# Kernel optimization log

Measured on AMD Instinct MI355X. Metric: run time of the kernel, lower is better.

## Reference

```python
import jax, jax.numpy as jnp
import numpy as np

EPS = 1e-5
NUM_HEADS = 16

def layernorm(x, g, b):
    mu = jnp.mean(x, axis=-1, keepdims=True)
    var = jnp.mean(jnp.square(x - mu), axis=-1, keepdims=True)
    return (x - mu) * jax.lax.rsqrt(var + EPS) * g + b

def setup_inputs() -> dict:
    key = jax.random.key(0)
    ks = jax.random.split(key, 5)
    B, N, C = 2, 2048, 1024
    s_in = 1.0 / np.sqrt(C)
    return {
        "x": jax.random.normal(ks[0], (B, N, C), jnp.float32),
        "ln1_g": jnp.ones((C,), jnp.float32),
        "ln1_b": jnp.zeros((C,), jnp.float32),
        "w_qk": jax.random.normal(ks[1], (C, 2 * C), jnp.float32) * s_in,
        "w_v": jax.random.normal(ks[2], (C, C), jnp.float32) * s_in,
        "ln2_g": jnp.ones((C,), jnp.float32),
        "ln2_b": jnp.zeros((C,), jnp.float32),
        "w_proj": jax.random.normal(ks[3], (C, C), jnp.float32) * s_in,
        "b_proj": jnp.zeros((C,), jnp.float32),
    }

def reference(x, ln1_g, ln1_b, w_qk, w_v, ln2_g, ln2_b, w_proj, b_proj):
    B, N, C = x.shape
    H = NUM_HEADS
    hd = C // H
    scale = hd ** (-0.5)
    xn = layernorm(x, ln1_g, ln1_b)
    # qk: [B,N,2C] -> q,k each [B,H,N,hd]
    qk = (xn @ w_qk).reshape(B, N, 2, H, hd).transpose(2, 0, 3, 1, 4)
    q, k = qk[0], qk[1]
    v = (xn @ w_v).reshape(B, N, H, hd).transpose(0, 2, 1, 3)  # [B,H,N,hd]
    attn = jnp.einsum("bhqd,bhkd->bhqk", q, k) * scale
    attn = jax.nn.softmax(attn, axis=-1)
    out = jnp.einsum("bhqk,bhkd->bhqd", attn, v)  # [B,H,N,hd]
    out = out.transpose(0, 2, 1, 3).reshape(B, N, C)
    out = layernorm(out, ln2_g, ln2_b)
    return out @ w_proj + b_proj
```

## Files before the change

kernel.cpp:

```cpp
#include <hip/hip_runtime.h>
#include <hip/hip_bf16.h>


typedef __attribute__((ext_vector_type(8))) short short8;
typedef __attribute__((ext_vector_type(4))) short short4v;
typedef __attribute__((ext_vector_type(4))) float float4v;
typedef __attribute__((ext_vector_type(4))) unsigned uint4v;

__device__ __forceinline__ unsigned short f2bf(float f) {
    unsigned u = __builtin_bit_cast(unsigned, f);
    return (unsigned short)((u + 0x7FFFu + ((u >> 16) & 1u)) >> 16);
}
__device__ __forceinline__ unsigned packbf2(float lo, float hi) {
    return __builtin_amdgcn_perm(__builtin_bit_cast(unsigned, hi) + 0x8000u,
                                 __builtin_bit_cast(unsigned, lo) + 0x8000u,
                                 0x07060302u);
}
__device__ __forceinline__ void gll16(const unsigned short* g, unsigned short* l) {
    __builtin_amdgcn_global_load_lds(
        (const __attribute__((address_space(1))) unsigned int*)g,
        (__attribute__((address_space(3))) unsigned int*)l, 16, 0, 0);
}

__global__ __launch_bounds__(256) void prep(
    const float* __restrict__ x, const float* __restrict__ g1, const float* __restrict__ b1,
    const float* __restrict__ w_qk, const float* __restrict__ w_v,
    const float* __restrict__ w_proj, const float* __restrict__ g2,
    const float* __restrict__ b2,
    unsigned short* __restrict__ xn, unsigned short* __restrict__ wqkvT,
    unsigned short* __restrict__ wgT, float* __restrict__ u, float* __restrict__ w0) {
    __shared__ float sh[32 * 33];
    const int bid = blockIdx.x, tid = threadIdx.x;
    if (bid < 4096) {
        const float4 v = reinterpret_cast<const float4*>(x + (size_t)bid * 1024)[tid];
        float s  = v.x + v.y + v.z + v.w;
        float sq = v.x * v.x + v.y * v.y + v.z * v.z + v.w * v.w;
#pragma unroll
        for (int off = 32; off >= 1; off >>= 1) {
            s  += __shfl_xor(s, off, 64);
            sq += __shfl_xor(sq, off, 64);
        }
        const int w = tid >> 6, lane = tid & 63;
        if (lane == 0) { sh[w] = s; sh[4 + w] = sq; }
        __syncthreads();
        s  = sh[0] + sh[1] + sh[2] + sh[3];
        sq = sh[4] + sh[5] + sh[6] + sh[7];
        const float mu = s * (1.f / 1024.f);
        const float rstd = rsqrtf(sq * (1.f / 1024.f) - mu * mu + 1e-5f);
        const float4 gv = reinterpret_cast<const float4*>(g1)[tid];
        const float4 bv = reinterpret_cast<const float4*>(b1)[tid];
        ushort4 o;
        o.x = f2bf((v.x - mu) * rstd * gv.x + bv.x);
        o.y = f2bf((v.y - mu) * rstd * gv.y + bv.y);
        o.z = f2bf((v.z - mu) * rstd * gv.z + bv.z);
        o.w = f2bf((v.w - mu) * rstd * gv.w + bv.w);
        *reinterpret_cast<ushort4*>(&xn[(size_t)bid * 1024 + tid * 4]) = o;
    } else {
        const float* in; unsigned short* out; int Cc, bx, by; bool doU = false;
        if (bid < 6144)      { int t = bid - 4096; in = w_qk;   out = wqkvT;               Cc = 2048; bx = t & 63; by = t >> 6; }
        else if (bid < 7168) { int t = bid - 6144; in = w_v;    out = wqkvT + 2048 * 1024; Cc = 1024; bx = t & 31; by = t >> 5; }
        else                 { int t = bid - 7168; in = w_proj; out = wgT; doU = true;     Cc = 1024; bx = t & 31; by = t >> 5; }
        const int c0 = bx * 32, r0 = by * 32;
        const int tx = tid & 31, ty = tid >> 5;
#pragma unroll
        for (int i = 0; i < 32; i += 8)
            sh[(ty + i) * 33 + tx] = in[(size_t)(r0 + ty + i) * Cc + c0 + tx];
        __syncthreads();
        const float scale = doU ? g2[r0 + tx] : 1.f;
        const float b2v   = doU ? b2[r0 + tx] : 0.f;
#pragma unroll
        for (int i = 0; i < 32; i += 8) {
            const float raw = sh[tx * 33 + ty + i];
            const float sc  = raw * scale;
            out[(size_t)(c0 + ty + i) * 1024 + r0 + tx] = f2bf(sc);
            if (doU) {
                float pu = sc, pw = raw * b2v;
#pragma unroll
                for (int off = 1; off <= 16; off <<= 1) {
                    pu += __shfl_xor(pu, off, 64);
                    pw += __shfl_xor(pw, off, 64);
                }
                if (tx == 0) {
                    atomicAdd(&u[c0 + ty + i], pu);
                    atomicAdd(&w0[c0 + ty + i], pw);
                }
            }
        }
    }
}

__global__ __launch_bounds__(512) void gemm256_qkv(const unsigned short* __restrict__ A,
                                                   const unsigned short* __restrict__ Bt,
                                                   unsigned short* __restrict__ qb,
                                                   unsigned short* __restrict__ kb,
                                                   unsigned short* __restrict__ vT) {
    __shared__ unsigned short As[2 * 256 * 64], Bs[2 * 256 * 64];
    const int tid = threadIdx.x, lane = tid & 63, w = tid >> 6;
    const int wm = (w >> 2) * 128, wn = (w & 3) * 64;
    const int quad = lane >> 4, l16 = lane & 15;
    const int ls = lane >> 3, sg = lane & 7;
    const int m0 = blockIdx.y * 256, n0 = blockIdx.x * 256;

    float4v acc[8][4];
#pragma unroll
    for (int mi = 0; mi < 8; mi++)
#pragma unroll
        for (int ni = 0; ni < 4; ni++) acc[mi][ni] = float4v{0.f, 0.f, 0.f, 0.f};

    const int g = (sg ^ ls) * 8;
#pragma unroll 1
    for (int s = -1; s < 16; s++) {
        if (s >= 0) __syncthreads();
        if (s + 1 < 16) {
            const int k0 = (s + 1) << 6, buf = ((s + 1) & 1) << 14;
            unsigned short* Ad = As + buf;
            unsigned short* Bd = Bs + buf;
#pragma unroll
            for (int i = 0; i < 4; i++) {
                const int r = w * 32 + i * 8 + ls;
                gll16(&A[(size_t)(m0 + r) * 1024 + k0 + g], &Ad[(w * 32 + i * 8) * 64]);
                gll16(&Bt[(size_t)(n0 + r) * 1024 + k0 + g], &Bd[(w * 32 + i * 8) * 64]);
            }
        }
        if (s < 0) continue;
        const unsigned short* Ac = As + ((s & 1) << 14);
        const unsigned short* Bc = Bs + ((s & 1) << 14);
#pragma unroll
        for (int ks = 0; ks < 2; ks++) {
            short8 af[8], bfr[4];
#pragma unroll
            for (int mi = 0; mi < 8; mi++) {
                const int r = wm + mi * 16 + l16;
                af[mi] = *reinterpret_cast<const short8*>(
                    &Ac[r * 64 + ((ks * 4 + quad) ^ (r & 7)) * 8]);
            }
#pragma unroll
            for (int ni = 0; ni < 4; ni++) {
                const int r = wn + ni * 16 + l16;
                bfr[ni] = *reinterpret_cast<const short8*>(
                    &Bc[r * 64 + ((ks * 4 + quad) ^ (r & 7)) * 8]);
            }
#pragma unroll
            for (int mi = 0; mi < 8; mi++)
#pragma unroll
                for (int ni = 0; ni < 4; ni++)
                    acc[mi][ni] = __builtin_amdgcn_mfma_f32_16x16x32_bf16(
                        af[mi], bfr[ni], acc[mi][ni], 0, 0, 0);
        }
    }

    const float QSCALE = 0.125f * 1.4426950408889634f;
#pragma unroll
    for (int mi = 0; mi < 8; mi++) {
        const int row0 = m0 + wm + mi * 16 + quad * 4;
        const int b = row0 >> 11, nq = row0 & 2047;
#pragma unroll
        for (int ni = 0; ni < 4; ni++) {
            const int col = n0 + wn + ni * 16 + l16;
            if (col < 1024) {
                const int h = col >> 6, d = col & 63;
#pragma unroll
                for (int r = 0; r < 4; r++)
                    qb[(((size_t)b * 16 + h) * 2048 + nq + r) * 64 + d] =
                        f2bf(acc[mi][ni][r] * QSCALE);
            } else if (col < 2048) {
                const int c = col - 1024, h = c >> 6, d = c & 63;
#pragma unroll
                for (int r = 0; r < 4; r++)
                    kb[(((size_t)b * 16 + h) * 2048 + nq + r) * 64 + d] = f2bf(acc[mi][ni][r]);
            } else {
                const int c = col - 2048, h = c >> 6, d = c & 63;
                const short4v sv = {(short)f2bf(acc[mi][ni][0]), (short)f2bf(acc[mi][ni][1]),
                                    (short)f2bf(acc[mi][ni][2]), (short)f2bf(acc[mi][ni][3])};
                *reinterpret_cast<short4v*>(
                    &vT[(((size_t)b * 16 + h) * 64 + d) * 2048 + nq]) = sv;
            }
        }
    }
}

__global__ __launch_bounds__(256) void flash_attn(const unsigned short* __restrict__ qbuf,
                                                  const unsigned short* __restrict__ kb,
                                                  const unsigned short* __restrict__ vT,
                                                  unsigned short* __restrict__ attn,
                                                  float2* __restrict__ part) {
    __shared__ unsigned short Ks[2][64 * 64];
    const int tid = threadIdx.x, lane = tid & 63, w = tid >> 6;
    const int quad = lane >> 4, l16 = lane & 15;
    const int ls = lane >> 3, sg = lane & 7;
    const int q0 = blockIdx.x * 128, bh = blockIdx.y;
    const size_t nbase = (size_t)bh * 2048;

    int srow[2];
#pragma unroll
    for (int i = 0; i < 2; i++) {
        const int pr = w * 16 + i * 8 + ls;
        srow[i] = (pr & 32) | ((pr & 12) << 1) | ((pr & 16) >> 2) | (pr & 3);
    }
    const int sgran = (sg ^ ls) << 3;

    short8 bq[2][2];
#pragma unroll
    for (int q2 = 0; q2 < 2; q2++)
#pragma unroll
        for (int ks = 0; ks < 2; ks++)
            bq[q2][ks] = *reinterpret_cast<const short8*>(
                &qbuf[(nbase + q0 + w * 32 + q2 * 16 + l16) * 64 + ks * 32 + quad * 8]);

    float l_part[2] = {0.f, 0.f};
    float4v o_acc[2][4];
#pragma unroll
    for (int q2 = 0; q2 < 2; q2++)
#pragma unroll
        for (int db = 0; db < 4; db++) o_acc[q2][db] = float4v{0.f, 0.f, 0.f, 0.f};

#pragma unroll
    for (int i = 0; i < 2; i++)
        gll16(&kb[(nbase + srow[i]) * 64 + sgran], &Ks[0][(w * 16 + i * 8) * 64]);

#pragma unroll 1
    for (int s = 0; s < 32; s++) {
        const int kt0 = s << 6;
        __syncthreads();
        if (s + 1 < 32) {
            const int ktn = (s + 1) << 6;
#pragma unroll
            for (int i = 0; i < 2; i++)
                gll16(&kb[(nbase + ktn + srow[i]) * 64 + sgran],
                      &Ks[(s + 1) & 1][(w * 16 + i * 8) * 64]);
        }
        short8 va[2][4];
#pragma unroll
        for (int k2 = 0; k2 < 2; k2++)
#pragma unroll
            for (int db = 0; db < 4; db++)
                va[k2][db] = *reinterpret_cast<const short8*>(
                    &vT[((size_t)bh * 64 + db * 16 + l16) * 2048 + kt0 + k2 * 32 + quad * 8]);

        const unsigned short* Kc = Ks[s & 1];
        short8 kf[2][4];
#pragma unroll
        for (int ks = 0; ks < 2; ks++)
#pragma unroll
            for (int cb = 0; cb < 4; cb++) {
                const int r = cb * 16 + l16;
                kf[ks][cb] = *reinterpret_cast<const short8*>(
                    &Kc[r * 64 + ((ks * 4 + quad) ^ (r & 7)) * 8]);
            }

#pragma unroll
        for (int q2 = 0; q2 < 2; q2++) {
            float4v s_acc[4];
#pragma unroll
            for (int cb = 0; cb < 4; cb++) s_acc[cb] = float4v{0.f, 0.f, 0.f, 0.f};
#pragma unroll
            for (int ks = 0; ks < 2; ks++)
#pragma unroll
                for (int cb = 0; cb < 4; cb++)
                    s_acc[cb] = __builtin_amdgcn_mfma_f32_16x16x32_bf16(
                        kf[ks][cb], bq[q2][ks], s_acc[cb], 0, 0, 0);

            float ls2 = 0.f;
            short8 pb[2];
#pragma unroll
            for (int k2 = 0; k2 < 2; k2++) {
                float p[8];
#pragma unroll
                for (int cc = 0; cc < 2; cc++)
#pragma unroll
                    for (int r = 0; r < 4; r++) {
                        const float pv = __builtin_amdgcn_exp2f(s_acc[k2 * 2 + cc][r]);
                        p[cc * 4 + r] = pv;
                        ls2 += pv;
                    }
                uint4v pd;
                pd.x = packbf2(p[0], p[1]); pd.y = packbf2(p[2], p[3]);
                pd.z = packbf2(p[4], p[5]); pd.w = packbf2(p[6], p[7]);
                pb[k2] = __builtin_bit_cast(short8, pd);
            }
            l_part[q2] += ls2;
#pragma unroll
            for (int k2 = 0; k2 < 2; k2++)
#pragma unroll
                for (int db = 0; db < 4; db++)
                    o_acc[q2][db] = __builtin_amdgcn_mfma_f32_16x16x32_bf16(
                        va[k2][db], pb[k2], o_acc[q2][db], 0, 0, 0);
        }
    }

    const int b = bh >> 4, h = bh & 15;
#pragma unroll
    for (int q2 = 0; q2 < 2; q2++) {
        float lr = l_part[q2];
        lr += __shfl_xor(lr, 16, 64);
        lr += __shfl_xor(lr, 32, 64);
        const float inv = 1.f / lr;
        const int grow = b * 2048 + q0 + w * 32 + q2 * 16 + l16;
        float s = 0.f, s2 = 0.f;
#pragma unroll
        for (int db = 0; db < 4; db++) {
            const float o0 = o_acc[q2][db][0] * inv, o1 = o_acc[q2][db][1] * inv;
            const float o2 = o_acc[q2][db][2] * inv, o3 = o_acc[q2][db][3] * inv;
            const ushort4 st = {f2bf(o0), f2bf(o1), f2bf(o2), f2bf(o3)};
            *reinterpret_cast<ushort4*>(
                &attn[(size_t)grow * 1024 + h * 64 + db * 16 + quad * 4]) = st;
            s  += (o0 + o1) + (o2 + o3);
            s2 += (o0 * o0 + o1 * o1) + (o2 * o2 + o3 * o3);
        }
        s  += __shfl_xor(s, 16, 64);  s  += __shfl_xor(s, 32, 64);
        s2 += __shfl_xor(s2, 16, 64); s2 += __shfl_xor(s2, 32, 64);
        if (quad == 0) part[(size_t)grow * 16 + h] = float2{s, s2};
    }
}

__device__ __forceinline__ void stage_tiles(const unsigned short* __restrict__ A,
                                            const unsigned short* __restrict__ Bt,
                                            int K, int m0, int n0, int k0,
                                            unsigned short* As, unsigned short* Bs,
                                            int w, int ls, int sg) {
#pragma unroll
    for (int i = 0; i < 4; i++) {
        const int r = w * 32 + i * 8 + ls;
        const int g = (sg ^ ls) * 8;
        gll16(&A[(size_t)(m0 + r) * K + k0 + g], &As[(w * 32 + i * 8) * 64]);
        gll16(&Bt[(size_t)(n0 + r) * K + k0 + g], &Bs[(w * 32 + i * 8) * 64]);
    }
}

__device__ __forceinline__ void gemm128_core(const unsigned short* __restrict__ A,
                                             const unsigned short* __restrict__ Bt,
                                             int K, int m0, int n0,
                                             unsigned short* As, unsigned short* Bs,
                                             float4v acc[4][4]) {
    const int tid = threadIdx.x, lane = tid & 63, w = tid >> 6;
    const int wr = (w >> 1) * 64, wc = (w & 1) * 64;
    const int quad = lane >> 4, l16 = lane & 15;
    const int ls = lane >> 3, sg = lane & 7;
#pragma unroll
    for (int mi = 0; mi < 4; mi++)
#pragma unroll
        for (int ni = 0; ni < 4; ni++) acc[mi][ni] = float4v{0.f, 0.f, 0.f, 0.f};

    const int NS = K >> 6;
    stage_tiles(A, Bt, K, m0, n0, 0, As, Bs, w, ls, sg);
    for (int s = 0; s < NS; s++) {
        __syncthreads();
        const int cur = (s & 1) << 13;
        if (s + 1 < NS)
            stage_tiles(A, Bt, K, m0, n0, (s + 1) << 6,
                        As + (((s + 1) & 1) << 13), Bs + (((s + 1) & 1) << 13),
                        w, ls, sg);
        const unsigned short* Ac = As + cur;
        const unsigned short* Bc = Bs + cur;
#pragma unroll
        for (int ks = 0; ks < 2; ks++) {
            short8 af[4], bfr[4];
#pragma unroll
            for (int mi = 0; mi < 4; mi++) {
                const int r = wr + mi * 16 + l16;
                af[mi] = *reinterpret_cast<const short8*>(
                    &Ac[r * 64 + ((ks * 4 + quad) ^ (r & 7)) * 8]);
            }
#pragma unroll
            for (int ni = 0; ni < 4; ni++) {
                const int r = wc + ni * 16 + l16;
                bfr[ni] = *reinterpret_cast<const short8*>(
                    &Bc[r * 64 + ((ks * 4 + quad) ^ (r & 7)) * 8]);
            }
#pragma unroll
            for (int mi = 0; mi < 4; mi++)
#pragma unroll
                for (int ni = 0; ni < 4; ni++)
                    acc[mi][ni] = __builtin_amdgcn_mfma_f32_16x16x32_bf16(
                        af[mi], bfr[ni], acc[mi][ni], 0, 0, 0);
        }
    }
}

__global__ __launch_bounds__(256) void gemm128_proj(const unsigned short* __restrict__ A,
                                                    const unsigned short* __restrict__ Bt,
                                                    const float2* __restrict__ part,
                                                    const float* __restrict__ u,
                                                    const float* __restrict__ w0,
                                                    const float* __restrict__ bias,
                                                    float* __restrict__ out) {
    __shared__ unsigned short As[2 * 128 * 64], Bs[2 * 128 * 64];
    __shared__ float2 rstat_s[128];
    const int m0 = blockIdx.y * 128, n0 = blockIdx.x * 128;
    {
        const int t = threadIdx.x, rloc = t >> 1, half = t & 1;
        const float4* p4 = reinterpret_cast<const float4*>(part);
        float s = 0.f, s2 = 0.f;
#pragma unroll
        for (int j = 0; j < 4; j++) {
            const float4 p = p4[(size_t)(m0 + rloc) * 8 + half * 4 + j];
            s += p.x + p.z; s2 += p.y + p.w;
        }
        s  += __shfl_xor(s, 1, 64);
        s2 += __shfl_xor(s2, 1, 64);
        if (!half) {
            const float mu = s * (1.f / 1024.f);
            const float rstd = rsqrtf(s2 * (1.f / 1024.f) - mu * mu + 1e-5f);
            rstat_s[rloc] = float2{rstd, mu * rstd};
        }
    }
    float4v acc[4][4];
    gemm128_core(A, Bt, 1024, m0, n0, As, Bs, acc);
    const int lane = threadIdx.x & 63, w = threadIdx.x >> 6;
    const int wr = (w >> 1) * 64, wc = (w & 1) * 64;
    const int quad = lane >> 4, l16 = lane & 15;
#pragma unroll
    for (int mi = 0; mi < 4; mi++) {
        const int rl0 = wr + mi * 16 + quad * 4;
        float2 rs[4];
#pragma unroll
        for (int r = 0; r < 4; r++) rs[r] = rstat_s[rl0 + r];
#pragma unroll
        for (int ni = 0; ni < 4; ni++) {
            const int col = n0 + wc + ni * 16 + l16;
            const float uu = u[col], ww = w0[col] + bias[col];
#pragma unroll
            for (int r = 0; r < 4; r++)
                out[(size_t)(m0 + rl0 + r) * 1024 + col] =
                    fmaf(rs[r].x, acc[mi][ni][r], ww - rs[r].y * uu);
        }
    }
}

extern "C" void kernel_launch(void* const* d_in, const int* in_sizes, int n_in,
                              void* d_out, int out_size, void* d_ws, size_t ws_size,
                              hipStream_t stream) {
    const float* x      = (const float*)d_in[0];
    const float* ln1_g  = (const float*)d_in[1];
    const float* ln1_b  = (const float*)d_in[2];
    const float* w_qk   = (const float*)d_in[3];
    const float* w_v    = (const float*)d_in[4];
    const float* ln2_g  = (const float*)d_in[5];
    const float* ln2_b  = (const float*)d_in[6];
    const float* w_proj = (const float*)d_in[7];
    const float* b_proj = (const float*)d_in[8];
    float* out = (float*)d_out;

    char* ws = (char*)d_ws;
    unsigned short* xn      = (unsigned short*)(ws + 0);
    unsigned short* wqkvT   = (unsigned short*)(ws + 8388608);
    unsigned short* wgT     = (unsigned short*)(ws + 14680064);
    unsigned short* qbuf    = (unsigned short*)(ws + 16777216);
    unsigned short* kbuf    = (unsigned short*)(ws + 25165824);
    unsigned short* vTbuf   = (unsigned short*)(ws + 33554432);
    unsigned short* attn    = (unsigned short*)(ws + 41943040);
    float2*         part    = (float2*)(ws + 50331648);
    float*          u       = (float*)(ws + 50888704);
    float*          w0      = (float*)(ws + 50892800);

    hipMemsetAsync(ws + 50888704, 0, 8192, stream);
    prep<<<8192, 256, 0, stream>>>(x, ln1_g, ln1_b, w_qk, w_v, w_proj, ln2_g, ln2_b,
                                   xn, wqkvT, wgT, u, w0);
    gemm256_qkv<<<dim3(12, 16), 512, 0, stream>>>(xn, wqkvT, qbuf, kbuf, vTbuf);
    flash_attn<<<dim3(16, 32), 256, 0, stream>>>(qbuf, kbuf, vTbuf, attn, part);
    gemm128_proj<<<dim3(8, 32), 256, 0, stream>>>(attn, wgT, part, u, w0, b_proj, out);
}
```

Measured before the change: 230.0 us.

## Stage V tiles in LDS for flash attention and retile projection GEMM

The flash attention kernel now loads V tiles into LDS through async global-to-LDS copies with a swizzled layout, as it already did for K. It processes two 64-key sub-tiles per barrier, so there are 16 iterations instead of 32. This replaces per-iteration uncoalesced direct global loads of V and halves the synchronisation count, at the cost of four times the LDS per block. The projection GEMM switches to 128x64 tiles, which doubles the grid to 512 blocks for better CU occupancy. The p row-sum is also reassociated into a tree.

```diff
diff --git a/kernel.cpp b/kernel.cpp
--- a/kernel.cpp
+++ b/kernel.cpp
@@ -184,7 +184,8 @@
                                                   const unsigned short* __restrict__ vT,
                                                   unsigned short* __restrict__ attn,
                                                   float2* __restrict__ part) {
-    __shared__ unsigned short Ks[2][64 * 64];
+    __shared__ unsigned short Ks[2][2][64 * 64];
+    __shared__ unsigned short Vs[2][2][64 * 64];
     const int tid = threadIdx.x, lane = tid & 63, w = tid >> 6;
     const int quad = lane >> 4, l16 = lane & 15;
     const int ls = lane >> 3, sg = lane & 7;
@@ -215,76 +216,91 @@
         for (int db = 0; db < 4; db++) o_acc[q2][db] = float4v{0.f, 0.f, 0.f, 0.f};
 
 #pragma unroll
-    for (int i = 0; i < 2; i++)
-        gll16(&kb[(nbase + srow[i]) * 64 + sgran], &Ks[0][(w * 16 + i * 8) * 64]);
+    for (int t = 0; t < 2; t++)
+#pragma unroll
+        for (int i = 0; i < 2; i++) {
+            gll16(&kb[(nbase + t * 64 + srow[i]) * 64 + sgran],
+                  &Ks[0][t][(w * 16 + i * 8) * 64]);
+            gll16(&vT[((size_t)bh * 64 + w * 16 + i * 8 + ls) * 2048 + t * 64 + sgran],
+                  &Vs[0][t][(w * 16 + i * 8) * 64]);
+        }
 
 #pragma unroll 1
-    for (int s = 0; s < 32; s++) {
-        const int kt0 = s << 6;
+    for (int s = 0; s < 16; s++) {
         __syncthreads();
-        if (s + 1 < 32) {
-            const int ktn = (s + 1) << 6;
-#pragma unroll
-            for (int i = 0; i < 2; i++)
-                gll16(&kb[(nbase + ktn + srow[i]) * 64 + sgran],
-                      &Ks[(s + 1) & 1][(w * 16 + i * 8) * 64]);
-        }
-        short8 va[2][4];
-#pragma unroll
-        for (int k2 = 0; k2 < 2; k2++)
-#pragma unroll
-            for (int db = 0; db < 4; db++)
-                va[k2][db] = *reinterpret_cast<const short8*>(
-                    &vT[((size_t)bh * 64 + db * 16 + l16) * 2048 + kt0 + k2 * 32 + quad * 8]);
-
-        const unsigned short* Kc = Ks[s & 1];
-        short8 kf[2][4];
-#pragma unroll
-        for (int ks = 0; ks < 2; ks++)
-#pragma unroll
-            for (int cb = 0; cb < 4; cb++) {
-                const int r = cb * 16 + l16;
-                kf[ks][cb] = *reinterpret_cast<const short8*>(
-                    &Kc[r * 64 + ((ks * 4 + quad) ^ (r & 7)) * 8]);
-            }
-
-#pragma unroll
-        for (int q2 = 0; q2 < 2; q2++) {
-            float4v s_acc[4];
-#pragma unroll
-            for (int cb = 0; cb < 4; cb++) s_acc[cb] = float4v{0.f, 0.f, 0.f, 0.f};
+        if (s + 1 < 16) {
+            const int ktn = (s + 1) << 7, buf = (s + 1) & 1;
+#pragma unroll
+            for (int t = 0; t < 2; t++)
+#pragma unroll
+                for (int i = 0; i < 2; i++) {
+                    gll16(&kb[(nbase + ktn + t * 64 + srow[i]) * 64 + sgran],
+                          &Ks[buf][t][(w * 16 + i * 8) * 64]);
+                    gll16(&vT[((size_t)bh * 64 + w * 16 + i * 8 + ls) * 2048 + ktn + t * 64 + sgran],
+                          &Vs[buf][t][(w * 16 + i * 8) * 64]);
+                }
+        }
+#pragma unroll
+        for (int t = 0; t < 2; t++) {
+            const unsigned short* Kc = Ks[s & 1][t];
+            const unsigned short* Vc = Vs[s & 1][t];
+
+            short8 kf[2][4];
 #pragma unroll
             for (int ks = 0; ks < 2; ks++)
 #pragma unroll
-                for (int cb = 0; cb < 4; cb++)
-                    s_acc[cb] = __builtin_amdgcn_mfma_f32_16x16x32_bf16(
-                        kf[ks][cb], bq[q2][ks], s_acc[cb], 0, 0, 0);
-
-            float ls2 = 0.f;
-            short8 pb[2];
-#pragma unroll
-            for (int k2 = 0; k2 < 2; k2++) {
-                float p[8];
-#pragma unroll
-                for (int cc = 0; cc < 2; cc++)
-#pragma unroll
-                    for (int r = 0; r < 4; r++) {
-                        const float pv = __builtin_amdgcn_exp2f(s_acc[k2 * 2 + cc][r]);
-                        p[cc * 4 + r] = pv;
-                        ls2 += pv;
-                    }
-                uint4v pd;
-                pd.x = packbf2(p[0], p[1]); pd.y = packbf2(p[2], p[3]);
-                pd.z = packbf2(p[4], p[5]); pd.w = packbf2(p[6], p[7]);
-                pb[k2] = __builtin_bit_cast(short8, pd);
-            }
-            l_part[q2] += ls2;
+                for (int cb = 0; cb < 4; cb++) {
+                    const int r = cb * 16 + l16;
+                    kf[ks][cb] = *reinterpret_cast<const short8*>(
+                        &Kc[r * 64 + ((ks * 4 + quad) ^ (r & 7)) * 8]);
+                }
+            short8 va[2][4];
 #pragma unroll
             for (int k2 = 0; k2 < 2; k2++)
 #pragma unroll
-                for (int db = 0; db < 4; db++)
-                    o_acc[q2][db] = __builtin_amdgcn_mfma_f32_16x16x32_bf16(
-                        va[k2][db], pb[k2], o_acc[q2][db], 0, 0, 0);
+                for (int db = 0; db < 4; db++) {
+                    const int r = db * 16 + l16;
+                    va[k2][db] = *reinterpret_cast<const short8*>(
+                        &Vc[r * 64 + ((k2 * 4 + quad) ^ (r & 7)) * 8]);
+                }
+
+#pragma unroll
+            for (int q2 = 0; q2 < 2; q2++) {
+                float4v s_acc[4];
+#pragma unroll
+                for (int cb = 0; cb < 4; cb++) s_acc[cb] = float4v{0.f, 0.f, 0.f, 0.f};
+#pragma unroll
+                for (int ks = 0; ks < 2; ks++)
+#pragma unroll
+                    for (int cb = 0; cb < 4; cb++)
+                        s_acc[cb] = __builtin_amdgcn_mfma_f32_16x16x32_bf16(
+                            kf[ks][cb], bq[q2][ks], s_acc[cb], 0, 0, 0);
+
+                float ls2 = 0.f;
+                short8 pb[2];
+#pragma unroll
+                for (int k2 = 0; k2 < 2; k2++) {
+                    float p[8];
+#pragma unroll
+                    for (int cc = 0; cc < 2; cc++)
+#pragma unroll
+                        for (int r = 0; r < 4; r++)
+                            p[cc * 4 + r] = __builtin_amdgcn_exp2f(s_acc[k2 * 2 + cc][r]);
+                    ls2 += ((p[0] + p[1]) + (p[2] + p[3])) +
+                           ((p[4] + p[5]) + (p[6] + p[7]));
+                    uint4v pd;
+                    pd.x = packbf2(p[0], p[1]); pd.y = packbf2(p[2], p[3]);
+                    pd.z = packbf2(p[4], p[5]); pd.w = packbf2(p[6], p[7]);
+                    pb[k2] = __builtin_bit_cast(short8, pd);
+                }
+                l_part[q2] += ls2;
+#pragma unroll
+                for (int k2 = 0; k2 < 2; k2++)
+#pragma unroll
+                    for (int db = 0; db < 4; db++)
+                        o_acc[q2][db] = __builtin_amdgcn_mfma_f32_16x16x32_bf16(
+                            va[k2][db], pb[k2], o_acc[q2][db], 0, 0, 0);
+            }
         }
     }
 
@@ -313,82 +329,22 @@
     }
 }
 
-__device__ __forceinline__ void stage_tiles(const unsigned short* __restrict__ A,
-                                            const unsigned short* __restrict__ Bt,
-                                            int K, int m0, int n0, int k0,
-                                            unsigned short* As, unsigned short* Bs,
-                                            int w, int ls, int sg) {
-#pragma unroll
-    for (int i = 0; i < 4; i++) {
-        const int r = w * 32 + i * 8 + ls;
-        const int g = (sg ^ ls) * 8;
-        gll16(&A[(size_t)(m0 + r) * K + k0 + g], &As[(w * 32 + i * 8) * 64]);
-        gll16(&Bt[(size_t)(n0 + r) * K + k0 + g], &Bs[(w * 32 + i * 8) * 64]);
-    }
-}
-
-__device__ __forceinline__ void gemm128_core(const unsigned short* __restrict__ A,
-                                             const unsigned short* __restrict__ Bt,
-                                             int K, int m0, int n0,
-                                             unsigned short* As, unsigned short* Bs,
-                                             float4v acc[4][4]) {
+__global__ __launch_bounds__(256) void gemm_proj(const unsigned short* __restrict__ A,
+                                                 const unsigned short* __restrict__ Bt,
+                                                 const float2* __restrict__ part,
+                                                 const float* __restrict__ u,
+                                                 const float* __restrict__ w0,
+                                                 const float* __restrict__ bias,
+                                                 float* __restrict__ out) {
+    __shared__ unsigned short As[2 * 128 * 64];
+    __shared__ unsigned short Bs[2 * 64 * 64];
+    __shared__ float2 rstat_s[128];
     const int tid = threadIdx.x, lane = tid & 63, w = tid >> 6;
-    const int wr = (w >> 1) * 64, wc = (w & 1) * 64;
     const int quad = lane >> 4, l16 = lane & 15;
     const int ls = lane >> 3, sg = lane & 7;
-#pragma unroll
-    for (int mi = 0; mi < 4; mi++)
-#pragma unroll
-        for (int ni = 0; ni < 4; ni++) acc[mi][ni] = float4v{0.f, 0.f, 0.f, 0.f};
-
-    const int NS = K >> 6;
-    stage_tiles(A, Bt, K, m0, n0, 0, As, Bs, w, ls, sg);
-    for (int s = 0; s < NS; s++) {
-        __syncthreads();
-        const int cur = (s & 1) << 13;
-        if (s + 1 < NS)
-            stage_tiles(A, Bt, K, m0, n0, (s + 1) << 6,
-                        As + (((s + 1) & 1) << 13), Bs + (((s + 1) & 1) << 13),
-                        w, ls, sg);
-        const unsigned short* Ac = As + cur;
-        const unsigned short* Bc = Bs + cur;
-#pragma unroll
-        for (int ks = 0; ks < 2; ks++) {
-            short8 af[4], bfr[4];
-#pragma unroll
-            for (int mi = 0; mi < 4; mi++) {
-                const int r = wr + mi * 16 + l16;
-                af[mi] = *reinterpret_cast<const short8*>(
-                    &Ac[r * 64 + ((ks * 4 + quad) ^ (r & 7)) * 8]);
-            }
-#pragma unroll
-            for (int ni = 0; ni < 4; ni++) {
-                const int r = wc + ni * 16 + l16;
-                bfr[ni] = *reinterpret_cast<const short8*>(
-                    &Bc[r * 64 + ((ks * 4 + quad) ^ (r & 7)) * 8]);
-            }
-#pragma unroll
-            for (int mi = 0; mi < 4; mi++)
-#pragma unroll
-                for (int ni = 0; ni < 4; ni++)
-                    acc[mi][ni] = __builtin_amdgcn_mfma_f32_16x16x32_bf16(
-                        af[mi], bfr[ni], acc[mi][ni], 0, 0, 0);
-        }
-    }
-}
-
-__global__ __launch_bounds__(256) void gemm128_proj(const unsigned short* __restrict__ A,
-                                                    const unsigned short* __restrict__ Bt,
-                                                    const float2* __restrict__ part,
-                                                    const float* __restrict__ u,
-                                                    const float* __restrict__ w0,
-                                                    const float* __restrict__ bias,
-                                                    float* __restrict__ out) {
-    __shared__ unsigned short As[2 * 128 * 64], Bs[2 * 128 * 64];
-    __shared__ float2 rstat_s[128];
-    const int m0 = blockIdx.y * 128, n0 = blockIdx.x * 128;
+    const int m0 = blockIdx.y * 128, n0 = blockIdx.x * 64;
     {
-        const int t = threadIdx.x, rloc = t >> 1, half = t & 1;
+        const int rloc = tid >> 1, half = tid & 1;
         const float4* p4 = reinterpret_cast<const float4*>(part);
         float s = 0.f, s2 = 0.f;
 #pragma unroll
@@ -404,20 +360,72 @@
             rstat_s[rloc] = float2{rstd, mu * rstd};
         }
     }
-    float4v acc[4][4];
-    gemm128_core(A, Bt, 1024, m0, n0, As, Bs, acc);
-    const int lane = threadIdx.x & 63, w = threadIdx.x >> 6;
-    const int wr = (w >> 1) * 64, wc = (w & 1) * 64;
-    const int quad = lane >> 4, l16 = lane & 15;
-#pragma unroll
-    for (int mi = 0; mi < 4; mi++) {
-        const int rl0 = wr + mi * 16 + quad * 4;
+
+    float4v acc[2][4];
+#pragma unroll
+    for (int mi = 0; mi < 2; mi++)
+#pragma unroll
+        for (int ni = 0; ni < 4; ni++) acc[mi][ni] = float4v{0.f, 0.f, 0.f, 0.f};
+
+    const int g = (sg ^ ls) * 8;
+#pragma unroll
+    for (int i = 0; i < 4; i++)
+        gll16(&A[(size_t)(m0 + w * 32 + i * 8 + ls) * 1024 + g], &As[(w * 32 + i * 8) * 64]);
+#pragma unroll
+    for (int i = 0; i < 2; i++)
+        gll16(&Bt[(size_t)(n0 + w * 16 + i * 8 + ls) * 1024 + g], &Bs[(w * 16 + i * 8) * 64]);
+
+#pragma unroll 1
+    for (int s = 0; s < 16; s++) {
+        __syncthreads();
+        if (s + 1 < 16) {
+            const int k0 = (s + 1) << 6;
+            unsigned short* Ad = As + (((s + 1) & 1) << 13);
+            unsigned short* Bd = Bs + (((s + 1) & 1) << 12);
+#pragma unroll
+            for (int i = 0; i < 4; i++)
+                gll16(&A[(size_t)(m0 + w * 32 + i * 8 + ls) * 1024 + k0 + g],
+                      &Ad[(w * 32 + i * 8) * 64]);
+#pragma unroll
+            for (int i = 0; i < 2; i++)
+                gll16(&Bt[(size_t)(n0 + w * 16 + i * 8 + ls) * 1024 + k0 + g],
+                      &Bd[(w * 16 + i * 8) * 64]);
+        }
+        const unsigned short* Ac = As + ((s & 1) << 13);
+        const unsigned short* Bc = Bs + ((s & 1) << 12);
+#pragma unroll
+        for (int ks = 0; ks < 2; ks++) {
+            short8 af[2], bfr[4];
+#pragma unroll
+            for (int mi = 0; mi < 2; mi++) {
+                const int r = w * 32 + mi * 16 + l16;
+                af[mi] = *reinterpret_cast<const short8*>(
+                    &Ac[r * 64 + ((ks * 4 + quad) ^ (r & 7)) * 8]);
+            }
+#pragma unroll
+            for (int ni = 0; ni < 4; ni++) {
+                const int r = ni * 16 + l16;
+                bfr[ni] = *reinterpret_cast<const short8*>(
+                    &Bc[r * 64 + ((ks * 4 + quad) ^ (r & 7)) * 8]);
+            }
+#pragma unroll
+            for (int mi = 0; mi < 2; mi++)
+#pragma unroll
+                for (int ni = 0; ni < 4; ni++)
+                    acc[mi][ni] = __builtin_amdgcn_mfma_f32_16x16x32_bf16(
+                        af[mi], bfr[ni], acc[mi][ni], 0, 0, 0);
+        }
+    }
+
+#pragma unroll
+    for (int mi = 0; mi < 2; mi++) {
+        const int rl0 = w * 32 + mi * 16 + quad * 4;
         float2 rs[4];
 #pragma unroll
         for (int r = 0; r < 4; r++) rs[r] = rstat_s[rl0 + r];
 #pragma unroll
         for (int ni = 0; ni < 4; ni++) {
-            const int col = n0 + wc + ni * 16 + l16;
+            const int col = n0 + ni * 16 + l16;
             const float uu = u[col], ww = w0[col] + bias[col];
 #pragma unroll
             for (int r = 0; r < 4; r++)
@@ -458,5 +466,5 @@
                                    xn, wqkvT, wgT, u, w0);
     gemm256_qkv<<<dim3(12, 16), 512, 0, stream>>>(xn, wqkvT, qbuf, kbuf, vTbuf);
     flash_attn<<<dim3(16, 32), 256, 0, stream>>>(qbuf, kbuf, vTbuf, attn, part);
-    gemm128_proj<<<dim3(8, 32), 256, 0, stream>>>(attn, wgT, part, u, w0, b_proj, out);
-}
+    gemm_proj<<<dim3(16, 32), 256, 0, stream>>>(attn, wgT, part, u, w0, b_proj, out);
+}
```

Result: faster. 202.0 us (-12.2%).
